# Performance work log

Hardware: AMD Instinct MI355X
Metric: run time of the kernel (lower is better)

## Reference

```python
import jax, jax.numpy as jnp
import numpy as np

NUM_HEADS = 8
HEAD_SPLITS = [2, 3, 3]          # heads per window size
WINDOWS = [3, 5, 7]


def _dwconv(x, w, b, k):
    """Depthwise 2D conv, SAME padding. x:[B,C,H,W], w:[C,1,k,k], b:[C]."""
    p = k // 2
    y = jax.lax.conv_general_dilated(
        x, w, window_strides=(1, 1), padding=[(p, p), (p, p)],
        dimension_numbers=("NCHW", "OIHW", "NCHW"),
        feature_group_count=x.shape[1])
    return y + b[None, :, None, None]


def setup_inputs() -> dict:
    key = jax.random.key(0)
    ks = jax.random.split(key, 8)
    B, N, C = 8, 3137, 768
    c = C // NUM_HEADS  # 96
    inp = {
        "x": jax.random.normal(ks[0], (B, N, C), dtype=jnp.float32),
        "qkv_w": jax.random.normal(ks[1], (3 * C, C), dtype=jnp.float32) * 0.02,
        "qkv_b": jnp.zeros((3 * C,), dtype=jnp.float32),
        "proj_w": jax.random.normal(ks[2], (C, C), dtype=jnp.float32) * 0.02,
        "proj_b": jnp.zeros((C,), dtype=jnp.float32),
        "conv3_w": jax.random.normal(ks[3], (2 * c, 1, 3, 3), dtype=jnp.float32) * 0.02,
        "conv3_b": jnp.zeros((2 * c,), dtype=jnp.float32),
        "conv5_w": jax.random.normal(ks[4], (3 * c, 1, 5, 5), dtype=jnp.float32) * 0.02,
        "conv5_b": jnp.zeros((3 * c,), dtype=jnp.float32),
        "conv7_w": jax.random.normal(ks[5], (3 * c, 1, 7, 7), dtype=jnp.float32) * 0.02,
        "conv7_b": jnp.zeros((3 * c,), dtype=jnp.float32),
        "H": 56,
        "W": 56,
    }
    return inp


def reference(x, qkv_w, qkv_b, proj_w, proj_b,
              conv3_w, conv3_b, conv5_w, conv5_b, conv7_w, conv7_b, H, W):
    B, N, C = x.shape
    h = NUM_HEADS
    c = C // h
    scale = c ** -0.5

    # qkv projection -> q,k,v each [B,h,N,c]
    qkv = x @ qkv_w.T + qkv_b
    qkv = qkv.reshape(B, N, 3, h, c).transpose(2, 0, 3, 1, 4)
    q, k, v = qkv[0], qkv[1], qkv[2]

    # factorized attention: softmax over token axis of k
    k_softmax = jax.nn.softmax(k, axis=2)
    kv = jnp.einsum("bhnc,bhnd->bhcd", k_softmax, v)       # [B,h,c,c]
    factor_att = jnp.einsum("bhnc,bhcd->bhnd", q, kv)      # [B,h,N,c]

    # ConvRelPosEnc on image tokens
    q_img = q[:, :, 1:, :]                                  # [B,h,HW,c]
    v_img = v[:, :, 1:, :]                                  # [B,h,HW,c]
    v_img = v_img.transpose(0, 1, 3, 2).reshape(B, h * c, H, W)
    splits = np.cumsum([s * c for s in HEAD_SPLITS])[:-1].tolist()
    v2, v5, v7 = jnp.split(v_img, splits, axis=1)
    conv_v = jnp.concatenate([
        _dwconv(v2, conv3_w, conv3_b, 3),
        _dwconv(v5, conv5_w, conv5_b, 5),
        _dwconv(v7, conv7_w, conv7_b, 7),
    ], axis=1)                                              # [B,h*c,H,W]
    conv_v = conv_v.reshape(B, h, c, H * W).transpose(0, 1, 3, 2)  # [B,h,HW,c]
    ev = q_img * conv_v
    crpe = jnp.pad(ev, ((0, 0), (0, 0), (1, 0), (0, 0)))    # zero row for cls token

    out = scale * factor_att + crpe                         # [B,h,N,c]
    out = out.transpose(0, 2, 1, 3).reshape(B, N, C)
    out = out @ proj_w.T + proj_b
    return out
```

## Files before the change

kernel.cpp:

```cpp
#include <hip/hip_runtime.h>
#include <hip/hip_bf16.h>


#define BB 8
#define NN 3137
#define HH 8
#define CH 96
#define HW 3136
#define IMG 56
#define MTOK (BB*NN)
#define NCHK 16
#define CTOK 197

typedef __bf16 bf16x8 __attribute__((ext_vector_type(8)));
typedef unsigned short u16x8 __attribute__((ext_vector_type(8)));
typedef unsigned short u16x4 __attribute__((ext_vector_type(4)));
typedef float  f32x4  __attribute__((ext_vector_type(4)));
typedef float  f32x8  __attribute__((ext_vector_type(8)));

__device__ __forceinline__ void gl_lds16(const void* g, void* l) {
    __builtin_amdgcn_global_load_lds(
        (const __attribute__((address_space(1))) unsigned int*)g,
        (__attribute__((address_space(3))) unsigned int*)l, 16, 0, 0);
}
__device__ __forceinline__ void memfence_bar() {
    asm volatile("" ::: "memory");
    __builtin_amdgcn_s_barrier();
    asm volatile("" ::: "memory");
}

__global__ __launch_bounds__(256) void cvt_bf16(
    const float* __restrict__ in, unsigned short* __restrict__ out, int n8)
{
    const int i = blockIdx.x * 256 + threadIdx.x;
    if (i < n8) {
        const f32x8 v = ((const f32x8*)in)[i];
        ((u16x8*)out)[i] = (u16x8)__builtin_convertvector(v, bf16x8);
    }
}

__global__ __launch_bounds__(512, 2) void gemm256(
    const unsigned short* __restrict__ A,
    const unsigned short* __restrict__ W,
    const float* __restrict__ bias,
    unsigned short* __restrict__ C,
    int lda, int ldw, int ldc, int M, int NT)
{
    __shared__ alignas(16) unsigned short lds[2*2*2*8192];
    const int tid = threadIdx.x;
    const int nwg = gridDim.x * gridDim.y;
    const int orig = blockIdx.y * gridDim.x + blockIdx.x;
    const int q8 = nwg >> 3, r8 = nwg & 7;
    const int xcd = orig & 7, off = orig >> 3;
    const int wgid = (xcd < r8 ? xcd*(q8+1) : r8*(q8+1) + (xcd-r8)*q8) + off;
    const int n0 = (wgid % gridDim.x) * 256;
    const int m0 = (wgid / gridDim.x) * 256;

    const int lane = tid & 63, wave = tid >> 6;
    const int lr = lane & 15, quad = lane >> 4;
    const int wm2 = wave >> 2;
    const int wn4 = wave & 3;
    const int bh  = wn4 >> 1;
    const int brow = (wn4 & 1) * 64;

    const int srow0 = tid >> 3, skc0 = tid & 7;
    const int srow1 = (tid + 512) >> 3, skc1 = tid & 7;
    const int kce0 = (skc0 ^ (srow0 & 7)) * 8;
    const int kce1 = (skc1 ^ (srow1 & 7)) * 8;

    auto stage = [&](int p, int mat, int h, int t) {
        unsigned short* dst = lds + (((p*2 + mat)*2 + h) << 13);
        const int kb = t * 64;
        if (mat == 0) {
            int g0 = m0 + h*128 + srow0; if (g0 > M-1) g0 = M-1;
            int g1 = m0 + h*128 + srow1; if (g1 > M-1) g1 = M-1;
            gl_lds16(A + (size_t)g0*lda + kb + kce0, dst + tid*8);
            gl_lds16(A + (size_t)g1*lda + kb + kce1, dst + (tid+512)*8);
        } else {
            const int g0 = n0 + h*128 + srow0;
            const int g1 = n0 + h*128 + srow1;
            gl_lds16(W + (size_t)g0*ldw + kb + kce0, dst + tid*8);
            gl_lds16(W + (size_t)g1*ldw + kb + kce1, dst + (tid+512)*8);
        }
    };
    auto ldsrd = [&](const unsigned short* base, int rowh, int c16) -> bf16x8 {
        return *(const bf16x8*)(base + rowh*64 + ((c16 ^ (rowh & 7)) << 3));
    };

    stage(0,1,0,0); stage(0,1,1,0);
    stage(0,0,0,0); stage(0,0,1,0);
    stage(1,1,0,1); stage(1,1,1,1);
    asm volatile("s_waitcnt vmcnt(4)" ::: "memory");
    memfence_bar();

    f32x4 acc[8][4] = {};
    bf16x8 bfr[4][2], af[2][2];
    for (int t = 0; t < NT; ++t) {
        const int p = t & 1;
        const unsigned short* Abuf = lds + (((p*2 + 0)*2 + wm2) << 13);
        const unsigned short* Bbuf = lds + (((p*2 + 1)*2 + bh ) << 13);
#pragma unroll
        for (int q = 0; q < 4; ++q) {
            if (q == 0) {
#pragma unroll
                for (int j = 0; j < 4; ++j)
#pragma unroll
                    for (int ks = 0; ks < 2; ++ks)
                        bfr[j][ks] = ldsrd(Bbuf, brow + j*16 + lr, ks*4 + quad);
            }
#pragma unroll
            for (int ii = 0; ii < 2; ++ii)
#pragma unroll
                for (int ks = 0; ks < 2; ++ks)
                    af[ii][ks] = ldsrd(Abuf, q*32 + ii*16 + lr, ks*4 + quad);
            if (q == 0) { if (t+1 < NT) stage(p^1, 0, 0, t+1); }
            else if (q == 1) { if (t+1 < NT) stage(p^1, 0, 1, t+1); }
            else if (q == 2) { if (t+2 < NT) stage(p, 1, 0, t+2); }
            else             { if (t+2 < NT) stage(p, 1, 1, t+2); }
            __builtin_amdgcn_s_setprio(1);
#pragma unroll
            for (int ii = 0; ii < 2; ++ii)
#pragma unroll
                for (int j = 0; j < 4; ++j)
#pragma unroll
                    for (int ks = 0; ks < 2; ++ks)
                        acc[q*2+ii][j] = __builtin_amdgcn_mfma_f32_16x16x32_bf16(
                            bfr[j][ks], af[ii][ks], acc[q*2+ii][j], 0, 0, 0);
            __builtin_amdgcn_s_setprio(0);
            if (q == 3) {
                if (t+2 < NT)      asm volatile("s_waitcnt vmcnt(4)" ::: "memory");
                else if (t+1 < NT) asm volatile("s_waitcnt vmcnt(0)" ::: "memory");
            }
            memfence_bar();
        }
    }

#pragma unroll
    for (int i = 0; i < 8; ++i) {
        const int row = m0 + wm2*128 + i*16 + lr;
        if (row < M) {
#pragma unroll
            for (int j = 0; j < 4; ++j) {
                const int col = n0 + wn4*64 + j*16 + quad*4;
                const f32x4 bv = *(const f32x4*)(bias + col);
                u16x4 st;
#pragma unroll
                for (int r = 0; r < 4; ++r)
                    st[r] = __hip_bfloat16_raw(__float2bfloat16(acc[i][j][r] + bv[r])).x;
                *(u16x4*)&C[(size_t)row*ldc + col] = st;
            }
        }
    }
}

template<bool OUT_F32>
__global__ __launch_bounds__(256) void gemm_bt(
    const unsigned short* __restrict__ A, int lda,
    const unsigned short* __restrict__ W,
    const float* __restrict__ bias,
    void* __restrict__ Cptr, int ldc,
    int M, int Nd, int K)
{
    __shared__ alignas(16) unsigned short As[128*32];
    __shared__ alignas(16) unsigned short Bs[128*32];
    const int tid  = threadIdx.x;
    const int nwg = gridDim.x * gridDim.y;
    int orig = blockIdx.y * gridDim.x + blockIdx.x;
    const int q8 = nwg >> 3, r8 = nwg & 7;
    const int xcd = orig & 7, off = orig >> 3;
    const int wgid = (xcd < r8 ? xcd*(q8+1) : r8*(q8+1) + (xcd-r8)*q8) + off;
    const int n0   = (wgid % gridDim.x) * 128;
    const int m0   = (wgid / gridDim.x) * 128;
    const int lane = tid & 63;
    const int wave = tid >> 6;
    const int wm   = (wave >> 1) * 64;
    const int wn   = (wave & 1) * 64;
    const int lr   = lane & 15;
    const int quad = lane >> 4;

    const int r0 = tid >> 2, c0 = (tid & 3) * 8;
    const int r1 = r0 + 64;
    int am0 = m0 + r0; if (am0 > M-1) am0 = M-1;
    int am1 = m0 + r1; if (am1 > M-1) am1 = M-1;
    const unsigned short* a0 = A + (size_t)am0*lda + c0;
    const unsigned short* a1 = A + (size_t)am1*lda + c0;
    const unsigned short* w0 = W + (size_t)(n0+r0)*K + c0;
    const unsigned short* w1 = W + (size_t)(n0+r1)*K + c0;
    unsigned short* lA0 = As + tid*8;
    unsigned short* lA1 = As + (tid+256)*8;
    unsigned short* lB0 = Bs + tid*8;
    unsigned short* lB1 = Bs + (tid+256)*8;

    f32x4 acc[4][4] = {};
    for (int k0 = 0; k0 < K; k0 += 32) {
        __syncthreads();
        gl_lds16(a0 + k0, lA0);
        gl_lds16(a1 + k0, lA1);
        gl_lds16(w0 + k0, lB0);
        gl_lds16(w1 + k0, lB1);
        asm volatile("s_waitcnt vmcnt(0)" ::: "memory");
        __syncthreads();
        bf16x8 af[4], bfr[4];
#pragma unroll
        for (int i = 0; i < 4; ++i) {
            af[i]  = *(const bf16x8*)(As + (wm + i*16 + lr)*32 + quad*8);
            bfr[i] = *(const bf16x8*)(Bs + (wn + i*16 + lr)*32 + quad*8);
        }
#pragma unroll
        for (int i = 0; i < 4; ++i)
#pragma unroll
            for (int j = 0; j < 4; ++j)
                acc[i][j] = __builtin_amdgcn_mfma_f32_16x16x32_bf16(bfr[j], af[i], acc[i][j], 0, 0, 0);
    }
#pragma unroll
    for (int i = 0; i < 4; ++i) {
        const int row = m0 + wm + i*16 + lr;
        if (row < M) {
#pragma unroll
            for (int j = 0; j < 4; ++j) {
                const int col = n0 + wn + j*16 + quad*4;
                const f32x4 bv = *(const f32x4*)(bias + col);
                f32x4 v;
#pragma unroll
                for (int r = 0; r < 4; ++r) v[r] = acc[i][j][r] + bv[r];
                if (OUT_F32) {
                    *(f32x4*)&((float*)Cptr)[(size_t)row*ldc + col] = v;
                } else {
                    u16x4 st;
#pragma unroll
                    for (int r = 0; r < 4; ++r)
                        st[r] = __hip_bfloat16_raw(__float2bfloat16(v[r])).x;
                    *(u16x4*)&((__hip_bfloat16*)Cptr)[(size_t)row*ldc + col] = st;
                }
            }
        }
    }
}

__global__ __launch_bounds__(256) void kv_accum(
    const __hip_bfloat16* __restrict__ qkv,
    float* __restrict__ kvp,
    float* __restrict__ spart)
{
    const int bh = blockIdx.x;
    const int chunk = blockIdx.y;
    const int b = bh >> 3, h = bh & 7;
    const int nstart = chunk * CTOK;
    int nend = nstart + CTOK; if (nend > NN) nend = NN;
    __shared__ float krow[16][96], vrow[16][96];
    __shared__ float sacc[192][8];
    const int t = threadIdx.x;

    const int sr = t / 12, sc = (t % 12) * 8;
    const __hip_bfloat16* kb = qkv + (size_t)b*NN*2304 + 768 + h*96;
    const __hip_bfloat16* vb = kb + 768;
    float ssum[8] = {};

    const int ci = (t >> 4) * 6;
    const int di = (t & 15) * 6;
    float acc[6][6] = {};
    for (int n = nstart; n < nend; n += 16) {
        __syncthreads();
        if (t < 192) {
            const int nn = n + sr;
            if (nn < nend) {
                const bf16x8 kr = *(const bf16x8*)(kb + (size_t)nn*2304 + sc);
                const bf16x8 vr = *(const bf16x8*)(vb + (size_t)nn*2304 + sc);
                const f32x8 kf = __builtin_convertvector(kr, f32x8);
                const f32x8 vf = __builtin_convertvector(vr, f32x8);
                f32x8 ke;
#pragma unroll
                for (int j = 0; j < 8; ++j) { ke[j] = __expf(kf[j]); ssum[j] += ke[j]; }
                *(f32x4*)&krow[sr][sc]   = *(const f32x4*)&ke;
                *(f32x4*)&krow[sr][sc+4] = *((const f32x4*)&ke + 1);
                *(f32x4*)&vrow[sr][sc]   = *(const f32x4*)&vf;
                *(f32x4*)&vrow[sr][sc+4] = *((const f32x4*)&vf + 1);
            } else {
                const f32x4 z = {0.f,0.f,0.f,0.f};
                *(f32x4*)&krow[sr][sc] = z; *(f32x4*)&krow[sr][sc+4] = z;
                *(f32x4*)&vrow[sr][sc] = z; *(f32x4*)&vrow[sr][sc+4] = z;
            }
        }
        __syncthreads();
#pragma unroll 4
        for (int r = 0; r < 16; ++r) {
            float kf[6], vf[6];
#pragma unroll
            for (int i = 0; i < 6; ++i) kf[i] = krow[r][ci+i];
#pragma unroll
            for (int j = 0; j < 6; ++j) vf[j] = vrow[r][di+j];
#pragma unroll
            for (int i = 0; i < 6; ++i)
#pragma unroll
                for (int j = 0; j < 6; ++j)
                    acc[i][j] += kf[i] * vf[j];
        }
    }
    float* outp = kvp + (size_t)(chunk*64 + bh)*9216;
#pragma unroll
    for (int i = 0; i < 6; ++i)
#pragma unroll
        for (int j = 0; j < 6; ++j)
            outp[(ci+i)*96 + (di+j)] = acc[i][j];
    if (t < 192) {
#pragma unroll
        for (int j = 0; j < 8; ++j) sacc[t][j] = ssum[j];
    }
    __syncthreads();
    if (t < 96) {
        const int g = t >> 3, e = t & 7;
        float S = 0.f;
#pragma unroll
        for (int m = 0; m < 16; ++m) S += sacc[g + 12*m][e];
        spart[(size_t)(chunk*64 + bh)*96 + t] = S;
    }
}

__global__ __launch_bounds__(256) void kv_prep(
    const float* __restrict__ kvp, const float* __restrict__ spart,
    unsigned short* __restrict__ kvb)
{
    const int bh = blockIdx.x, y = blockIdx.y;
    __shared__ float sinv[24];
    const int t = threadIdx.x;
    const int cbase = y * 24;
    if (t < 24) {
        float S = 0.f;
#pragma unroll
        for (int ch = 0; ch < NCHK; ++ch)
            S += spart[(size_t)(ch*64 + bh)*96 + cbase + t];
        sinv[t] = 1.0f / S;
    }
    __syncthreads();
    unsigned short* dst = kvb + (size_t)bh*19968;
    for (int i = t; i < 2304; i += 256) {
        const int ii = y*2304 + i;
        const int c = ii / 96, d = ii % 96;
        float v = 0.f;
#pragma unroll
        for (int ch = 0; ch < NCHK; ++ch)
            v += kvp[(size_t)(ch*64 + bh)*9216 + ii];
        v *= sinv[c - cbase];
        const __hip_bfloat16 hb = __float2bfloat16(v);
        const float lo = v - __bfloat162float(hb);
        const __hip_bfloat16 lb = __float2bfloat16(lo);
        dst[d*104 + c]        = __hip_bfloat16_raw(hb).x;
        dst[9984 + d*104 + c] = __hip_bfloat16_raw(lb).x;
    }
}

__global__ __launch_bounds__(256) void fatt(
    const __hip_bfloat16* __restrict__ qkv,
    const unsigned short* __restrict__ kvb,
    const __hip_bfloat16* __restrict__ cv,
    __hip_bfloat16* __restrict__ att)
{
    __shared__ alignas(16) unsigned short kvs[2*96*104];
    const int tile = blockIdx.x, h = blockIdx.y, b = blockIdx.z;
    const int t = threadIdx.x, lane = t & 63, wave = t >> 6;
    const int lr = lane & 15, quad = lane >> 4;

    const unsigned short* kg = kvb + (size_t)(b*8 + h)*19968;
#pragma unroll
    for (int s = 0; s < 10; ++s) {
        const int slot = t + s*256;
        if (slot < 2496) gl_lds16(kg + slot*8, kvs + slot*8);
    }

    const int n0 = tile*128 + wave*32;
    const unsigned short* qbu = (const unsigned short*)qkv + (size_t)b*NN*2304 + h*96;
    bf16x8 af[2][3];
#pragma unroll
    for (int i = 0; i < 2; ++i) {
        int n = n0 + i*16 + lr; if (n > NN-1) n = NN-1;
#pragma unroll
        for (int kk = 0; kk < 3; ++kk)
            af[i][kk] = *(const bf16x8*)(qbu + (size_t)n*2304 + kk*32 + quad*8);
    }
    asm volatile("s_waitcnt vmcnt(0)" ::: "memory");
    __syncthreads();

    f32x4 acc[2][6] = {};
#pragma unroll
    for (int j = 0; j < 6; ++j) {
#pragma unroll
        for (int kk = 0; kk < 3; ++kk) {
            const bf16x8 bhh = *(const bf16x8*)(kvs + (j*16 + lr)*104 + kk*32 + quad*8);
            const bf16x8 bll = *(const bf16x8*)(kvs + 9984 + (j*16 + lr)*104 + kk*32 + quad*8);
#pragma unroll
            for (int i = 0; i < 2; ++i) {
                acc[i][j] = __builtin_amdgcn_mfma_f32_16x16x32_bf16(af[i][kk], bhh, acc[i][j], 0, 0, 0);
                acc[i][j] = __builtin_amdgcn_mfma_f32_16x16x32_bf16(af[i][kk], bll, acc[i][j], 0, 0, 0);
            }
        }
    }

    const float scale = 0.10206207261596577f;
    const __hip_bfloat16* qb  = (const __hip_bfloat16*)qbu;
    const __hip_bfloat16* cvb = cv + (size_t)(b*8 + h)*HW*96;
    __hip_bfloat16* ab = att + (size_t)b*NN*2304 + h*96;
#pragma unroll
    for (int i = 0; i < 2; ++i) {
#pragma unroll
        for (int j = 0; j < 6; ++j) {
            const int col = j*16 + lr;
#pragma unroll
            for (int r = 0; r < 4; ++r) {
                const int n = n0 + i*16 + quad*4 + r;
                if (n < NN) {
                    float v = scale * acc[i][j][r];
                    if (n > 0) {
                        const float qv = __bfloat162float(qb[(size_t)n*2304 + col]);
                        v += qv * __bfloat162float(cvb[(size_t)(n-1)*96 + col]);
                    }
                    ab[(size_t)n*2304 + col] = __float2bfloat16(v);
                }
            }
        }
    }
}

template<int KS>
__device__ __forceinline__ void dw_band(
    float (*vt)[64][36],
    const __hip_bfloat16* __restrict__ vbase,
    const float* __restrict__ wp, float bv,
    __hip_bfloat16* __restrict__ cvo,
    int y0)
{
    constexpr int P = KS/2;
    const int t = threadIdx.x;
    float wr[KS*KS];
#pragma unroll
    for (int i = 0; i < KS*KS; ++i) wr[i] = wp[i];

    const int spx = t >> 2, sc0 = (t & 3) * 8;
    const int ch = t & 31, xs = t >> 5;
    const int xbase = xs*7 + 4 - P;

#pragma unroll
    for (int r = -P; r < P; ++r) {
        const int y = y0 + r;
        if (t < 224) {
            f32x8 v8 = {0,0,0,0,0,0,0,0};
            if ((unsigned)y < (unsigned)IMG) {
                const bf16x8 rv = *(const bf16x8*)(vbase + (size_t)(y*IMG + spx)*2304 + sc0);
                v8 = __builtin_convertvector(rv, f32x8);
            }
            float* dst = &vt[(y+8)&7][spx+4][sc0];
            *(f32x4*)dst     = *(f32x4*)&v8;
            *(f32x4*)(dst+4) = *((f32x4*)&v8 + 1);
        }
    }

    for (int yy = y0; yy < y0 + 14; ++yy) {
        {
            const int y = yy + P;
            if (t < 224) {
                f32x8 v8 = {0,0,0,0,0,0,0,0};
                if ((unsigned)y < (unsigned)IMG) {
                    const bf16x8 rv = *(const bf16x8*)(vbase + (size_t)(y*IMG + spx)*2304 + sc0);
                    v8 = __builtin_convertvector(rv, f32x8);
                }
                float* dst = &vt[(y+8)&7][spx+4][sc0];
                *(f32x4*)dst     = *(f32x4*)&v8;
                *(f32x4*)(dst+4) = *((f32x4*)&v8 + 1);
            }
        }
        __syncthreads();
        float acc[7];
#pragma unroll
        for (int j = 0; j < 7; ++j) acc[j] = bv;
        for (int dy = 0; dy < KS; ++dy) {
            const float* rowp = &vt[(yy + dy - P + 8) & 7][0][ch] + xbase*36;
            float win[7 + 2*P];
#pragma unroll
            for (int i = 0; i < 7 + 2*P; ++i) win[i] = rowp[i*36];
#pragma unroll
            for (int dx = 0; dx < KS; ++dx)
#pragma unroll
                for (int j = 0; j < 7; ++j)
                    acc[j] += wr[dy*KS+dx] * win[j+dx];
        }
        const int p0 = yy*IMG + xs*7;
#pragma unroll
        for (int j = 0; j < 7; ++j)
            cvo[(size_t)(p0 + j)*96] = __float2bfloat16(acc[j]);
        __syncthreads();
    }
}

__global__ __launch_bounds__(256) void dwconv2(
    const __hip_bfloat16* __restrict__ qkv,
    const float* __restrict__ w3, const float* __restrict__ b3,
    const float* __restrict__ w5, const float* __restrict__ b5,
    const float* __restrict__ w7, const float* __restrict__ b7,
    __hip_bfloat16* __restrict__ cv)
{
    __shared__ float vt[8][64][36];
    const int band = blockIdx.x, grp = blockIdx.y, b = blockIdx.z;
    const int t = threadIdx.x;
    {
        const int s = t >> 5, i = t & 31;
        const int xi = i >> 2;
        const int xp = (xi < 4) ? xi : 56 + xi;
        const int c0 = (i & 3) * 8;
        const f32x4 z = {0.f, 0.f, 0.f, 0.f};
        *(f32x4*)&vt[s][xp][c0]     = z;
        *(f32x4*)&vt[s][xp][c0+4]   = z;
    }
    const int chbase = grp * 32;
    const int wg = chbase + (t & 31);
    const int h = wg / 96, d = wg % 96;
    const int y0 = band * 14;
    const __hip_bfloat16* vbase = qkv + (size_t)b*NN*2304 + 2304 + 1536 + chbase;
    __hip_bfloat16* cvo = cv + ((size_t)(b*8 + h)*HW)*96 + d;
    if (grp < 6)        dw_band<3>(vt, vbase, w3 + wg*9,        b3[wg],     cvo, y0);
    else if (grp < 15)  dw_band<5>(vt, vbase, w5 + (wg-192)*25, b5[wg-192], cvo, y0);
    else                dw_band<7>(vt, vbase, w7 + (wg-480)*49, b7[wg-480], cvo, y0);
}

extern "C" void kernel_launch(void* const* d_in, const int* in_sizes, int n_in,
                              void* d_out, int out_size, void* d_ws, size_t ws_size,
                              hipStream_t stream)
{
    const float* x      = (const float*)d_in[0];
    const float* qkv_w  = (const float*)d_in[1];
    const float* qkv_b  = (const float*)d_in[2];
    const float* proj_w = (const float*)d_in[3];
    const float* proj_b = (const float*)d_in[4];
    const float* w3 = (const float*)d_in[5];
    const float* b3 = (const float*)d_in[6];
    const float* w5 = (const float*)d_in[7];
    const float* b5 = (const float*)d_in[8];
    const float* w7 = (const float*)d_in[9];
    const float* b7 = (const float*)d_in[10];
    float* out = (float*)d_out;

    char* ws = (char*)d_ws;
    const size_t QKV_B = (size_t)MTOK * 2304 * 2;
    const size_t XB_B  = (size_t)MTOK * 768 * 2;
    const size_t SH_B  = XB_B;
    const size_t KV_B  = (size_t)64 * 9216 * 4;
    const size_t ST_B  = 49152;
    const size_t WB_B  = (size_t)2304 * 768 * 2;
    const size_t PW_B  = (size_t)768 * 768 * 2;
    if (ws_size < QKV_B + SH_B + KV_B + ST_B + WB_B + PW_B) return;
    __hip_bfloat16* qkv  = (__hip_bfloat16*)ws;
    unsigned short* xb   = (unsigned short*)(ws + QKV_B);
    float*          kvp  = (float*)(ws + QKV_B);
    float*          spart= (float*)(ws + QKV_B + (size_t)NCHK*64*9216*4);
    __hip_bfloat16* cv   = (__hip_bfloat16*)(ws + QKV_B);
    unsigned short* wb   = (unsigned short*)(ws + QKV_B + SH_B + KV_B + ST_B);
    unsigned short* pwb  = (unsigned short*)(ws + QKV_B + SH_B + KV_B + ST_B + WB_B);

    cvt_bf16<<<(MTOK*768/8 + 255)/256, 256, 0, stream>>>(x, xb, MTOK*768/8);
    cvt_bf16<<<(2304*768/8 + 255)/256, 256, 0, stream>>>(qkv_w, wb, 2304*768/8);
    cvt_bf16<<<(768*768/8 + 255)/256, 256, 0, stream>>>(proj_w, pwb, 768*768/8);
    gemm256<<<dim3(9, 99), 512, 0, stream>>>(
        xb, wb, qkv_b, (unsigned short*)qkv, 768, 768, 2304, MTOK, 768/64);
    kv_accum<<<dim3(64, NCHK), 256, 0, stream>>>(qkv, kvp, spart);
    kv_prep<<<dim3(64, 4), 256, 0, stream>>>(kvp, spart, wb);
    dwconv2<<<dim3(4, 24, 8), 256, 0, stream>>>(qkv, w3, b3, w5, b5, w7, b7, cv);
    fatt<<<dim3(25, 8, 8), 256, 0, stream>>>(qkv, wb, cv,
                                             (__hip_bfloat16*)ws + 768);
    gemm_bt<true><<<dim3(6, 197), 256, 0, stream>>>(
        (const unsigned short*)ws + 768, 2304, pwb, proj_b, out, 768,
        MTOK, 768, 768);
}
```

Before: 509.0 us.

## Use inline-asm LDS reads with precomputed swizzle and restructured barriers in GEMM

Replaces the C++ LDS fragment loads in the bf16 GEMM main loop with inline ds_read_b128 using precomputed byte addresses and swizzle offsets. It also drops the compiler memory-clobber fences around barriers and adds a second barrier per sub-step before an explicit lgkmcnt(0) wait and a sched_barrier. The aim is to cut address arithmetic and let LDS reads overlap the issue of the next global-to-LDS stage. The extra barrier and the hand-placed waits may add synchronization cost, and the missing memory clobbers could allow unsafe reordering.

```diff
diff --git a/kernel.cpp b/kernel.cpp
--- a/kernel.cpp
+++ b/kernel.cpp
@@ -23,10 +23,13 @@
         (const __attribute__((address_space(1))) unsigned int*)g,
         (__attribute__((address_space(3))) unsigned int*)l, 16, 0, 0);
 }
-__device__ __forceinline__ void memfence_bar() {
-    asm volatile("" ::: "memory");
-    __builtin_amdgcn_s_barrier();
-    asm volatile("" ::: "memory");
+__device__ __forceinline__ unsigned ldsaddr(const void* p) {
+    return (unsigned)(size_t)(const __attribute__((address_space(3))) char*)p;
+}
+__device__ __forceinline__ bf16x8 ds_rd128(unsigned a) {
+    bf16x8 r;
+    asm volatile("ds_read_b128 %0, %1" : "=v"(r) : "v"(a));
+    return r;
 }
 
 __global__ __launch_bounds__(256) void cvt_bf16(
@@ -83,40 +86,45 @@
             gl_lds16(W + (size_t)g1*ldw + kb + kce1, dst + (tid+512)*8);
         }
     };
-    auto ldsrd = [&](const unsigned short* base, int rowh, int c16) -> bf16x8 {
-        return *(const bf16x8*)(base + rowh*64 + ((c16 ^ (rowh & 7)) << 3));
-    };
+
+    const unsigned ldsB = ldsaddr(lds);
+    const unsigned swz0 = (unsigned)(((0*4 + quad) ^ (lr & 7)) << 4);
+    const unsigned swz1 = (unsigned)(((1*4 + quad) ^ (lr & 7)) << 4);
 
     stage(0,1,0,0); stage(0,1,1,0);
     stage(0,0,0,0); stage(0,0,1,0);
     stage(1,1,0,1); stage(1,1,1,1);
     asm volatile("s_waitcnt vmcnt(4)" ::: "memory");
-    memfence_bar();
+    __builtin_amdgcn_s_barrier();
 
     f32x4 acc[8][4] = {};
     bf16x8 bfr[4][2], af[2][2];
     for (int t = 0; t < NT; ++t) {
         const int p = t & 1;
-        const unsigned short* Abuf = lds + (((p*2 + 0)*2 + wm2) << 13);
-        const unsigned short* Bbuf = lds + (((p*2 + 1)*2 + bh ) << 13);
+        const unsigned Ab = ldsB + ((unsigned)((p*2 + 0)*2 + wm2) << 14) + (unsigned)lr*128;
+        const unsigned Bb = ldsB + ((unsigned)((p*2 + 1)*2 + bh ) << 14) + (unsigned)(brow + lr)*128;
 #pragma unroll
         for (int q = 0; q < 4; ++q) {
             if (q == 0) {
 #pragma unroll
-                for (int j = 0; j < 4; ++j)
-#pragma unroll
-                    for (int ks = 0; ks < 2; ++ks)
-                        bfr[j][ks] = ldsrd(Bbuf, brow + j*16 + lr, ks*4 + quad);
-            }
-#pragma unroll
-            for (int ii = 0; ii < 2; ++ii)
-#pragma unroll
-                for (int ks = 0; ks < 2; ++ks)
-                    af[ii][ks] = ldsrd(Abuf, q*32 + ii*16 + lr, ks*4 + quad);
-            if (q == 0) { if (t+1 < NT) stage(p^1, 0, 0, t+1); }
+                for (int j = 0; j < 4; ++j) {
+                    bfr[j][0] = ds_rd128(Bb + j*16*128 + swz0);
+                    bfr[j][1] = ds_rd128(Bb + j*16*128 + swz1);
+                }
+            }
+#pragma unroll
+            for (int ii = 0; ii < 2; ++ii) {
+                const unsigned ra = Ab + (q*32 + ii*16)*128;
+                af[ii][0] = ds_rd128(ra + swz0);
+                af[ii][1] = ds_rd128(ra + swz1);
+            }
+            if (q == 0)      { if (t+1 < NT) stage(p^1, 0, 0, t+1); }
             else if (q == 1) { if (t+1 < NT) stage(p^1, 0, 1, t+1); }
             else if (q == 2) { if (t+2 < NT) stage(p, 1, 0, t+2); }
             else             { if (t+2 < NT) stage(p, 1, 1, t+2); }
+            __builtin_amdgcn_s_barrier();
+            asm volatile("s_waitcnt lgkmcnt(0)" ::: "memory");
+            __builtin_amdgcn_sched_barrier(0);
             __builtin_amdgcn_s_setprio(1);
 #pragma unroll
             for (int ii = 0; ii < 2; ++ii)
@@ -131,7 +139,7 @@
                 if (t+2 < NT)      asm volatile("s_waitcnt vmcnt(4)" ::: "memory");
                 else if (t+1 < NT) asm volatile("s_waitcnt vmcnt(0)" ::: "memory");
             }
-            memfence_bar();
+            __builtin_amdgcn_s_barrier();
         }
     }
 
```

New measurement: 502.1 us. About the same (-1.4%).
